# Kernel tuning notes

Measured on AMD Instinct MI355X. Metric: run time of the kernel, lower is better.

The kernel has to match this reference:

```python
import jax, jax.numpy as jnp
import numpy as np

N, F, H, C, E, G = 100000, 128, 64, 2, 1000000, 1000

def setup_inputs() -> dict:
    key = jax.random.key(0)
    ks = jax.random.split(key, 12)
    x = jax.random.normal(ks[0], (N, F), dtype=jnp.float32)
    edge_index = jax.random.randint(ks[1], (2, E), 0, N, dtype=jnp.int64)
    batch = jnp.sort(jax.random.randint(ks[2], (N,), 0, G, dtype=jnp.int64))
    def lin(k, fan_in, fan_out):
        s = 1.0 / np.sqrt(fan_in)
        kw, kb = jax.random.split(k)
        W = jax.random.uniform(kw, (fan_in, fan_out), jnp.float32, -s, s)
        b = jax.random.uniform(kb, (fan_out,), jnp.float32, -s, s)
        return W, b
    W1a, b1a = lin(ks[3], F, H)
    W1b, b1b = lin(ks[4], H, H)
    W2a, b2a = lin(ks[5], H, H)
    W2b, b2b = lin(ks[6], H, H)
    Wf, bf = lin(ks[7], H, C)
    return {"x": x, "edge_index": edge_index, "batch": batch,
            "W1a": W1a, "b1a": b1a, "W1b": W1b, "b1b": b1b,
            "W2a": W2a, "b2a": b2a, "W2b": W2b, "b2b": b2b,
            "Wf": Wf, "bf": bf}

def reference(x, edge_index, batch, W1a, b1a, W1b, b1b, W2a, b2a, W2b, b2b, Wf, bf):
    src, dst = edge_index[0], edge_index[1]
    n = x.shape[0]

    def gin_conv(h, Wa, ba, Wb, bb):
        # sum-aggregate source features onto destination nodes (eps = 0)
        agg = jax.ops.segment_sum(h[src], dst, num_segments=n)
        z = h + agg  # (1 + eps) * h + agg, eps=0
        return jax.nn.relu(z @ Wa + ba) @ Wb + bb

    h = jax.nn.relu(gin_conv(x, W1a, b1a, W1b, b1b))
    h = jax.nn.relu(gin_conv(h, W2a, b2a, W2b, b2b))

    # global mean pool per graph
    sums = jax.ops.segment_sum(h, batch, num_segments=G)
    counts = jax.ops.segment_sum(jnp.ones((n,), h.dtype), batch, num_segments=G)
    pooled = sums / jnp.clip(counts, 1.0)[:, None]
    return pooled @ Wf + bf
```

## Files before the change

### kernel.cpp

```cpp
#include <hip/hip_runtime.h>

#define HD 64
#define CAP 32


typedef _Float16 half8 __attribute__((ext_vector_type(8)));
typedef float f32x4 __attribute__((ext_vector_type(4)));

__device__ __forceinline__ unsigned short f2h(float f) {
    _Float16 h = (_Float16)f;
    unsigned short u;
    __builtin_memcpy(&u, &h, 2);
    return u;
}
__device__ __forceinline__ float h2f(unsigned short u) {
    _Float16 h;
    __builtin_memcpy(&h, &u, 2);
    return (float)h;
}

__device__ __forceinline__ int swz(int row, int bytecol) {
    return row * 128 + (bytecol ^ ((row & 7) << 4));
}
__device__ __forceinline__ int swz256(int row, int bytecol) {
    return row * 256 + (bytecol ^ ((row & 7) << 4));
}

__device__ __forceinline__ half8 bfrag(const float* __restrict__ W,
                                       int kc, int ntbase, int lane) {
    const int col = ntbase + (lane & 15);
    const float* wc = W + (size_t)(kc * 32 + ((lane >> 4) << 3)) * HD + col;
    half8 b;
#pragma unroll
    for (int j = 0; j < 8; ++j) b[j] = (_Float16)wc[j * HD];
    return b;
}

__global__ __launch_bounds__(128) void gemm128_mfma(const float* __restrict__ X,
                                                    const float* __restrict__ W,
                                                    unsigned short* __restrict__ Y, int n) {
    __shared__ __align__(16) unsigned short Xs[32 * 128];
    char* XsB = (char*)Xs;

    const int lane  = threadIdx.x & 63;
    const int wid   = threadIdx.x >> 6;
    const int row0  = blockIdx.x * 32;
    const int rbase = wid * 16;
    const int qo    = lane & 15;
    const int kg    = lane >> 4;

    const float4* Xg = (const float4*)X;
    for (int i = lane; i < 512; i += 64) {
        const int r   = i >> 5;
        const int c4  = i & 31;
        const int row = row0 + rbase + r;
        float4 v = make_float4(0.f, 0.f, 0.f, 0.f);
        if (row < n) v = Xg[(size_t)row * 32 + c4];
        ushort4 p;
        p.x = f2h(v.x); p.y = f2h(v.y); p.z = f2h(v.z); p.w = f2h(v.w);
        *(ushort4*)(XsB + swz256(rbase + r, c4 * 8)) = p;
    }

    const int arow = rbase + qo;
    half8 a[4];
#pragma unroll
    for (int kc = 0; kc < 4; ++kc)
        a[kc] = *(half8*)(XsB + swz256(arow, kc * 64 + kg * 16));

#pragma unroll
    for (int nt = 0; nt < 4; ++nt) {
        f32x4 c = (f32x4){0.f, 0.f, 0.f, 0.f};
#pragma unroll
        for (int kc = 0; kc < 4; ++kc)
            c = __builtin_amdgcn_mfma_f32_16x16x32_f16(a[kc], bfrag(W, kc, nt * 16, lane), c, 0, 0, 0);
#pragma unroll
        for (int j = 0; j < 4; ++j) {
            const int row = row0 + rbase + kg * 4 + j;
            if (row < n) Y[(size_t)row * HD + nt * 16 + qo] = f2h(c[j]);
        }
    }
}

__global__ __launch_bounds__(256) void fill_xcd(const int* __restrict__ src,
                                                const int* __restrict__ dst,
                                                int* __restrict__ fillpos,
                                                int* __restrict__ eidx,
                                                int E, int n) {
    const int xcd   = blockIdx.x & 7;
    const int chunk = blockIdx.x >> 3;
    const int nchk  = gridDim.x >> 3;
    const int cs    = (E + nchk - 1) / nchk;
    const int lo    = chunk * cs;
    const int hi    = min(lo + cs, E);
    const int nd8   = n >> 3;
    const int rlo   = xcd * nd8;
    const int rhi   = (xcd == 7) ? n : rlo + nd8;

    for (int t = lo + (int)threadIdx.x; t < hi; t += 256) {
        const int d = dst[t];
        if (d >= rlo && d < rhi) {
            const int p = atomicAdd(&fillpos[d], 1);
            if (p < CAP) eidx[(size_t)d * CAP + p] = src[t];
        }
    }
}

__device__ __forceinline__ void gather_pair(const unsigned short* __restrict__ Y,
                                            const int* __restrict__ deg,
                                            const int* __restrict__ eidx,
                                            int v0, int v1, int n, int lane,
                                            float4& A0, float4& A1) {
    const int sub = lane >> 4;
    const int qo  = lane & 15;
    const ushort4* Yq = (const ushort4*)Y;

    const int c0 = (v0 < n) ? min(deg[v0], CAP) : 0;
    const int c1 = (v1 < n) ? min(deg[v1], CAP) : 0;
    const int s0 = v0 * CAP;
    const int s1 = v1 * CAP;

    const int myu0 = (c0 > 0) ? eidx[s0 + min(lane, c0 - 1)] : 0;
    const int myu1 = (c1 > 0) ? eidx[s1 + min(lane, c1 - 1)] : 0;
    ushort4 self0 = make_ushort4(0, 0, 0, 0);
    ushort4 self1 = make_ushort4(0, 0, 0, 0);
    if (v0 < n && sub == 0) self0 = Yq[(size_t)v0 * 16 + qo];
    if (v1 < n && sub == 0) self1 = Yq[(size_t)v1 * 16 + qo];

    float4 a0 = make_float4(h2f(self0.x), h2f(self0.y), h2f(self0.z), h2f(self0.w));
    float4 a1 = make_float4(h2f(self1.x), h2f(self1.y), h2f(self1.z), h2f(self1.w));

    const int cmax = max(c0, c1);
#pragma unroll 1
    for (int i = 0; i < cmax; i += 16) {
        const int rem0 = c0 - i;
        const int rem1 = c1 - i;
        const int u00 = __shfl(myu0, i + 0  + sub);
        const int u01 = __shfl(myu0, i + 4  + sub);
        const int u02 = __shfl(myu0, i + 8  + sub);
        const int u03 = __shfl(myu0, i + 12 + sub);
        const int u10 = __shfl(myu1, i + 0  + sub);
        const int u11 = __shfl(myu1, i + 4  + sub);
        const int u12 = __shfl(myu1, i + 8  + sub);
        const int u13 = __shfl(myu1, i + 12 + sub);
        ushort4 f00 = make_ushort4(0,0,0,0), f01 = make_ushort4(0,0,0,0);
        ushort4 f02 = make_ushort4(0,0,0,0), f03 = make_ushort4(0,0,0,0);
        ushort4 f10 = make_ushort4(0,0,0,0), f11 = make_ushort4(0,0,0,0);
        ushort4 f12 = make_ushort4(0,0,0,0), f13 = make_ushort4(0,0,0,0);
        if (sub < rem0)      f00 = Yq[(size_t)u00 * 16 + qo];
        if (sub + 4 < rem0)  f01 = Yq[(size_t)u01 * 16 + qo];
        if (sub + 8 < rem0)  f02 = Yq[(size_t)u02 * 16 + qo];
        if (sub + 12 < rem0) f03 = Yq[(size_t)u03 * 16 + qo];
        if (sub < rem1)      f10 = Yq[(size_t)u10 * 16 + qo];
        if (sub + 4 < rem1)  f11 = Yq[(size_t)u11 * 16 + qo];
        if (sub + 8 < rem1)  f12 = Yq[(size_t)u12 * 16 + qo];
        if (sub + 12 < rem1) f13 = Yq[(size_t)u13 * 16 + qo];
        a0.x += (h2f(f00.x) + h2f(f01.x)) + (h2f(f02.x) + h2f(f03.x));
        a0.y += (h2f(f00.y) + h2f(f01.y)) + (h2f(f02.y) + h2f(f03.y));
        a0.z += (h2f(f00.z) + h2f(f01.z)) + (h2f(f02.z) + h2f(f03.z));
        a0.w += (h2f(f00.w) + h2f(f01.w)) + (h2f(f02.w) + h2f(f03.w));
        a1.x += (h2f(f10.x) + h2f(f11.x)) + (h2f(f12.x) + h2f(f13.x));
        a1.y += (h2f(f10.y) + h2f(f11.y)) + (h2f(f12.y) + h2f(f13.y));
        a1.z += (h2f(f10.z) + h2f(f11.z)) + (h2f(f12.z) + h2f(f13.z));
        a1.w += (h2f(f10.w) + h2f(f11.w)) + (h2f(f12.w) + h2f(f13.w));
    }

    a0.x += __shfl_xor(a0.x, 16); a0.y += __shfl_xor(a0.y, 16);
    a0.z += __shfl_xor(a0.z, 16); a0.w += __shfl_xor(a0.w, 16);
    a0.x += __shfl_xor(a0.x, 32); a0.y += __shfl_xor(a0.y, 32);
    a0.z += __shfl_xor(a0.z, 32); a0.w += __shfl_xor(a0.w, 32);
    a1.x += __shfl_xor(a1.x, 16); a1.y += __shfl_xor(a1.y, 16);
    a1.z += __shfl_xor(a1.z, 16); a1.w += __shfl_xor(a1.w, 16);
    a1.x += __shfl_xor(a1.x, 32); a1.y += __shfl_xor(a1.y, 32);
    a1.z += __shfl_xor(a1.z, 32); a1.w += __shfl_xor(a1.w, 32);
    A0 = a0;
    A1 = a1;
}

__global__ __launch_bounds__(128) void layer_mid(const unsigned short* __restrict__ Y,
                                                 const int* __restrict__ deg,
                                                 const int* __restrict__ eidx,
                                                 const float* __restrict__ bpre,
                                                 const float* __restrict__ Wb,
                                                 const float* __restrict__ bb,
                                                 const float* __restrict__ Wn,
                                                 unsigned short* __restrict__ Yout, int n) {
    __shared__ __align__(16) unsigned short Xs[32 * 64];
    char* XsB = (char*)Xs;

    const int lane  = threadIdx.x & 63;
    const int wid   = threadIdx.x >> 6;
    const int row0  = blockIdx.x * 32;
    const int rbase = wid * 16;
    const int qo    = lane & 15;
    const int kg    = lane >> 4;

    const float4 bp4 = ((const float4*)bpre)[qo];
#pragma unroll 1
    for (int rr = 0; rr < 16; rr += 2) {
        const int v0 = row0 + rbase + rr;
        float4 A0, A1;
        gather_pair(Y, deg, eidx, v0, v0 + 1, n, lane, A0, A1);
        if (lane < 16) {
            ushort4 p0, p1;
            p0.x = f2h(fmaxf(A0.x + bp4.x, 0.f));
            p0.y = f2h(fmaxf(A0.y + bp4.y, 0.f));
            p0.z = f2h(fmaxf(A0.z + bp4.z, 0.f));
            p0.w = f2h(fmaxf(A0.w + bp4.w, 0.f));
            p1.x = f2h(fmaxf(A1.x + bp4.x, 0.f));
            p1.y = f2h(fmaxf(A1.y + bp4.y, 0.f));
            p1.z = f2h(fmaxf(A1.z + bp4.z, 0.f));
            p1.w = f2h(fmaxf(A1.w + bp4.w, 0.f));
            *(ushort4*)(XsB + swz(rbase + rr, qo * 8)) = p0;
            *(ushort4*)(XsB + swz(rbase + rr + 1, qo * 8)) = p1;
        }
    }

    const int arow = rbase + qo;
    half8 a0 = *(half8*)(XsB + swz(arow, kg * 16));
    half8 a1 = *(half8*)(XsB + swz(arow, 64 + kg * 16));

    f32x4 acc[4];
#pragma unroll
    for (int nt = 0; nt < 4; ++nt) {
        acc[nt] = (f32x4){0.f, 0.f, 0.f, 0.f};
        acc[nt] = __builtin_amdgcn_mfma_f32_16x16x32_f16(a0, bfrag(Wb, 0, nt * 16, lane), acc[nt], 0, 0, 0);
        acc[nt] = __builtin_amdgcn_mfma_f32_16x16x32_f16(a1, bfrag(Wb, 1, nt * 16, lane), acc[nt], 0, 0, 0);
    }

#pragma unroll
    for (int nt = 0; nt < 4; ++nt) {
        const float bbv = bb[nt * 16 + qo];
#pragma unroll
        for (int j = 0; j < 4; ++j) {
            const float h = fmaxf(acc[nt][j] + bbv, 0.f);
            *(unsigned short*)(XsB + swz(rbase + kg * 4 + j, (nt * 16 + qo) * 2)) = f2h(h);
        }
    }

    a0 = *(half8*)(XsB + swz(arow, kg * 16));
    a1 = *(half8*)(XsB + swz(arow, 64 + kg * 16));

#pragma unroll
    for (int nt = 0; nt < 4; ++nt) {
        f32x4 c2 = (f32x4){0.f, 0.f, 0.f, 0.f};
        c2 = __builtin_amdgcn_mfma_f32_16x16x32_f16(a0, bfrag(Wn, 0, nt * 16, lane), c2, 0, 0, 0);
        c2 = __builtin_amdgcn_mfma_f32_16x16x32_f16(a1, bfrag(Wn, 1, nt * 16, lane), c2, 0, 0, 0);
#pragma unroll
        for (int j = 0; j < 4; ++j) {
            const int row = row0 + rbase + kg * 4 + j;
            if (row < n) Yout[(size_t)row * HD + nt * 16 + qo] = f2h(c2[j]);
        }
    }
}

__global__ __launch_bounds__(128) void layer_end(const unsigned short* __restrict__ Y,
                                                 const int* __restrict__ deg,
                                                 const int* __restrict__ eidx,
                                                 const float* __restrict__ bpre,
                                                 const float* __restrict__ Wb,
                                                 const float* __restrict__ bb,
                                                 const int* __restrict__ batch,
                                                 float* __restrict__ sums,
                                                 float* __restrict__ counts, int n) {
    __shared__ __align__(16) unsigned short Xs[32 * 64];
    char* XsB = (char*)Xs;

    const int lane  = threadIdx.x & 63;
    const int wid   = threadIdx.x >> 6;
    const int row0  = blockIdx.x * 32;
    const int rbase = wid * 16;
    const int qo    = lane & 15;
    const int kg    = lane >> 4;

    const float4 bp4 = ((const float4*)bpre)[qo];
#pragma unroll 1
    for (int rr = 0; rr < 16; rr += 2) {
        const int v0 = row0 + rbase + rr;
        float4 A0, A1;
        gather_pair(Y, deg, eidx, v0, v0 + 1, n, lane, A0, A1);
        if (lane < 16) {
            ushort4 p0, p1;
            p0.x = f2h(fmaxf(A0.x + bp4.x, 0.f));
            p0.y = f2h(fmaxf(A0.y + bp4.y, 0.f));
            p0.z = f2h(fmaxf(A0.z + bp4.z, 0.f));
            p0.w = f2h(fmaxf(A0.w + bp4.w, 0.f));
            p1.x = f2h(fmaxf(A1.x + bp4.x, 0.f));
            p1.y = f2h(fmaxf(A1.y + bp4.y, 0.f));
            p1.z = f2h(fmaxf(A1.z + bp4.z, 0.f));
            p1.w = f2h(fmaxf(A1.w + bp4.w, 0.f));
            *(ushort4*)(XsB + swz(rbase + rr, qo * 8)) = p0;
            *(ushort4*)(XsB + swz(rbase + rr + 1, qo * 8)) = p1;
        }
    }

    const int arow = rbase + qo;
    half8 a0 = *(half8*)(XsB + swz(arow, kg * 16));
    half8 a1 = *(half8*)(XsB + swz(arow, 64 + kg * 16));

#pragma unroll
    for (int nt = 0; nt < 4; ++nt) {
        f32x4 c = (f32x4){0.f, 0.f, 0.f, 0.f};
        c = __builtin_amdgcn_mfma_f32_16x16x32_f16(a0, bfrag(Wb, 0, nt * 16, lane), c, 0, 0, 0);
        c = __builtin_amdgcn_mfma_f32_16x16x32_f16(a1, bfrag(Wb, 1, nt * 16, lane), c, 0, 0, 0);
        const float bbv = bb[nt * 16 + qo];
#pragma unroll
        for (int j = 0; j < 4; ++j) {
            const float h = fmaxf(c[j] + bbv, 0.f);
            *(unsigned short*)(XsB + swz(rbase + kg * 4 + j, (nt * 16 + qo) * 2)) = f2h(h);
        }
    }

    const int vbase = row0 + rbase;
    int   curg = -1;
    float racc = 0.f;
    float rcnt = 0.f;
#pragma unroll 1
    for (int r = 0; r < 16; ++r) {
        const int v = vbase + r;
        int g = -1;
        if (v < n) g = batch[v];
        if (g != curg) {
            if (curg >= 0) {
                unsafeAtomicAdd(&sums[(size_t)curg * HD + lane], racc);
                if (lane == 0) unsafeAtomicAdd(&counts[curg], rcnt);
            }
            curg = g;
            racc = 0.f;
            rcnt = 0.f;
        }
        if (g >= 0) {
            racc += h2f(*(unsigned short*)(XsB + swz(rbase + r, lane * 2)));
            rcnt += 1.f;
        }
    }
    if (curg >= 0) {
        unsafeAtomicAdd(&sums[(size_t)curg * HD + lane], racc);
        if (lane == 0) unsafeAtomicAdd(&counts[curg], rcnt);
    }
}

__global__ __launch_bounds__(256) void final_linear(const float* __restrict__ sums,
                                                    const float* __restrict__ counts,
                                                    const float* __restrict__ Wf,
                                                    const float* __restrict__ bfv,
                                                    float* __restrict__ out, int G, int C) {
    const int t = blockIdx.x * 256 + threadIdx.x;
    if (t >= G * C) return;
    const int g = t / C;
    const int c = t - g * C;
    const float inv = 1.0f / fmaxf(counts[g], 1.0f);
    float acc = 0.f;
    for (int h = 0; h < HD; ++h) acc += sums[(size_t)g * HD + h] * Wf[h * C + c];
    out[t] = acc * inv + bfv[c];
}

extern "C" void kernel_launch(void* const* d_in, const int* in_sizes, int n_in,
                              void* d_out, int out_size, void* d_ws, size_t ws_size,
                              hipStream_t stream) {
    const float* x    = (const float*)d_in[0];
    const int*   ei   = (const int*)d_in[1];
    const int*   batc = (const int*)d_in[2];
    const float* W1a  = (const float*)d_in[3];
    const float* b1a  = (const float*)d_in[4];
    const float* W1b  = (const float*)d_in[5];
    const float* b1b  = (const float*)d_in[6];
    const float* W2a  = (const float*)d_in[7];
    const float* b2a  = (const float*)d_in[8];
    const float* W2b  = (const float*)d_in[9];
    const float* b2b  = (const float*)d_in[10];
    const float* Wf   = (const float*)d_in[11];
    const float* bfv  = (const float*)d_in[12];

    const int n = in_sizes[2];
    const int E = in_sizes[1] / 2;
    const int C = in_sizes[12];
    const int G = out_size / C;

    const int* src = ei;
    const int* dst = ei + E;

    unsigned short* yA = (unsigned short*)d_ws;
    unsigned short* yB = yA + (size_t)n * HD;
    float* sums    = (float*)(yB + (size_t)n * HD);
    float* counts  = sums + (size_t)G * HD;
    int*   fillpos = (int*)(counts + G);
    int*   eidx    = fillpos + n;

    const int layerGrid = (n + 31) / 32;
    const int NCHUNK    = 512;

    hipMemsetAsync(fillpos, 0, (size_t)n * sizeof(int), stream);
    fill_xcd<<<8 * NCHUNK, 256, 0, stream>>>(src, dst, fillpos, eidx, E, n);

    gemm128_mfma<<<layerGrid, 128, 0, stream>>>(x, W1a, yA, n);

    layer_mid<<<layerGrid, 128, 0, stream>>>(yA, fillpos, eidx,
                                             b1a, W1b, b1b, W2a, yB, n);

    hipMemsetAsync(sums, 0, (size_t)G * (HD + 1) * sizeof(float), stream);
    layer_end<<<layerGrid, 128, 0, stream>>>(yB, fillpos, eidx,
                                             b2a, W2b, b2b, batc, sums, counts, n);

    final_linear<<<(G * C + 255) / 256, 256, 0, stream>>>(sums, counts, Wf, bfv,
                                                          (float*)d_out, G, C);
}
```

Baseline: 158.8 us.

## Fuse edge fill, first GEMM and pool zeroing into one launch; gather four rows per wave

```diff
diff --git a/kernel.cpp b/kernel.cpp
--- a/kernel.cpp
+++ b/kernel.cpp
@@ -36,188 +36,191 @@
     return b;
 }
 
-__global__ __launch_bounds__(128) void gemm128_mfma(const float* __restrict__ X,
-                                                    const float* __restrict__ W,
-                                                    unsigned short* __restrict__ Y, int n) {
-    __shared__ __align__(16) unsigned short Xs[32 * 128];
+__global__ __launch_bounds__(256) void fused_pre(const int* __restrict__ src,
+                                                 const int* __restrict__ dst,
+                                                 int* __restrict__ fillpos,
+                                                 int* __restrict__ eidx, int E,
+                                                 const float* __restrict__ X,
+                                                 const float* __restrict__ W,
+                                                 unsigned short* __restrict__ Y, int n,
+                                                 float* __restrict__ zbuf, int ZN,
+                                                 int FB, int GB, int ZB) {
+    __shared__ __align__(16) unsigned short Xs[64 * 128];
     char* XsB = (char*)Xs;
 
-    const int lane  = threadIdx.x & 63;
-    const int wid   = threadIdx.x >> 6;
-    const int row0  = blockIdx.x * 32;
-    const int rbase = wid * 16;
-    const int qo    = lane & 15;
-    const int kg    = lane >> 4;
-
-    const float4* Xg = (const float4*)X;
-    for (int i = lane; i < 512; i += 64) {
-        const int r   = i >> 5;
-        const int c4  = i & 31;
-        const int row = row0 + rbase + r;
-        float4 v = make_float4(0.f, 0.f, 0.f, 0.f);
-        if (row < n) v = Xg[(size_t)row * 32 + c4];
-        ushort4 p;
-        p.x = f2h(v.x); p.y = f2h(v.y); p.z = f2h(v.z); p.w = f2h(v.w);
-        *(ushort4*)(XsB + swz256(rbase + r, c4 * 8)) = p;
-    }
-
-    const int arow = rbase + qo;
-    half8 a[4];
-#pragma unroll
-    for (int kc = 0; kc < 4; ++kc)
-        a[kc] = *(half8*)(XsB + swz256(arow, kc * 64 + kg * 16));
-
-#pragma unroll
-    for (int nt = 0; nt < 4; ++nt) {
-        f32x4 c = (f32x4){0.f, 0.f, 0.f, 0.f};
+    const int bid = blockIdx.x;
+    const int tid = threadIdx.x;
+
+    if (bid < FB) {
+        const int xcd   = bid & 7;
+        const int chunk = bid >> 3;
+        const int nchk  = FB >> 3;
+        const int cs    = (E + nchk - 1) / nchk;
+        const int lo    = chunk * cs;
+        const int hi    = min(lo + cs, E);
+        const int nd8   = n >> 3;
+        const int rlo   = xcd * nd8;
+        const int rhi   = (xcd == 7) ? n : rlo + nd8;
+
+        for (int t = lo + tid; t < hi; t += 256) {
+            const int d = dst[t];
+            if (d >= rlo && d < rhi) {
+                const int p = atomicAdd(&fillpos[d], 1);
+                if (p < CAP) eidx[(size_t)d * CAP + p] = src[t];
+            }
+        }
+        return;
+    }
+
+    if (bid < FB + GB) {
+        const int lane  = tid & 63;
+        const int wid   = tid >> 6;
+        const int row0  = (bid - FB) * 64;
+        const int rbase = wid * 16;
+        const int qo    = lane & 15;
+        const int kg    = lane >> 4;
+
+        const float4* Xg = (const float4*)X;
+        for (int i = lane; i < 512; i += 64) {
+            const int r   = i >> 5;
+            const int c4  = i & 31;
+            const int row = row0 + rbase + r;
+            float4 v = make_float4(0.f, 0.f, 0.f, 0.f);
+            if (row < n) v = Xg[(size_t)row * 32 + c4];
+            ushort4 p;
+            p.x = f2h(v.x); p.y = f2h(v.y); p.z = f2h(v.z); p.w = f2h(v.w);
+            *(ushort4*)(XsB + swz256(rbase + r, c4 * 8)) = p;
+        }
+
+        const int arow = rbase + qo;
+        half8 a[4];
 #pragma unroll
         for (int kc = 0; kc < 4; ++kc)
-            c = __builtin_amdgcn_mfma_f32_16x16x32_f16(a[kc], bfrag(W, kc, nt * 16, lane), c, 0, 0, 0);
-#pragma unroll
-        for (int j = 0; j < 4; ++j) {
-            const int row = row0 + rbase + kg * 4 + j;
-            if (row < n) Y[(size_t)row * HD + nt * 16 + qo] = f2h(c[j]);
-        }
-    }
-}
-
-__global__ __launch_bounds__(256) void fill_xcd(const int* __restrict__ src,
-                                                const int* __restrict__ dst,
-                                                int* __restrict__ fillpos,
-                                                int* __restrict__ eidx,
-                                                int E, int n) {
-    const int xcd   = blockIdx.x & 7;
-    const int chunk = blockIdx.x >> 3;
-    const int nchk  = gridDim.x >> 3;
-    const int cs    = (E + nchk - 1) / nchk;
-    const int lo    = chunk * cs;
-    const int hi    = min(lo + cs, E);
-    const int nd8   = n >> 3;
-    const int rlo   = xcd * nd8;
-    const int rhi   = (xcd == 7) ? n : rlo + nd8;
-
-    for (int t = lo + (int)threadIdx.x; t < hi; t += 256) {
-        const int d = dst[t];
-        if (d >= rlo && d < rhi) {
-            const int p = atomicAdd(&fillpos[d], 1);
-            if (p < CAP) eidx[(size_t)d * CAP + p] = src[t];
-        }
-    }
-}
-
-__device__ __forceinline__ void gather_pair(const unsigned short* __restrict__ Y,
-                                            const int* __restrict__ deg,
-                                            const int* __restrict__ eidx,
-                                            int v0, int v1, int n, int lane,
-                                            float4& A0, float4& A1) {
+            a[kc] = *(half8*)(XsB + swz256(arow, kc * 64 + kg * 16));
+
+#pragma unroll
+        for (int nt = 0; nt < 4; ++nt) {
+            f32x4 c = (f32x4){0.f, 0.f, 0.f, 0.f};
+#pragma unroll
+            for (int kc = 0; kc < 4; ++kc)
+                c = __builtin_amdgcn_mfma_f32_16x16x32_f16(a[kc], bfrag(W, kc, nt * 16, lane), c, 0, 0, 0);
+#pragma unroll
+            for (int j = 0; j < 4; ++j) {
+                const int row = row0 + rbase + kg * 4 + j;
+                if (row < n) Y[(size_t)row * HD + nt * 16 + qo] = f2h(c[j]);
+            }
+        }
+        return;
+    }
+
+    {
+        const int zb   = bid - FB - GB;
+        const int strd = ZB * 256;
+        for (int i = zb * 256 + tid; i < ZN; i += strd) zbuf[i] = 0.f;
+    }
+}
+
+__device__ __forceinline__ void gather_quad4(const unsigned short* __restrict__ Y,
+                                             const int* __restrict__ deg,
+                                             const int* __restrict__ eidx,
+                                             int v0, int n, int lane,
+                                             float4 A[4]) {
     const int sub = lane >> 4;
     const int qo  = lane & 15;
     const ushort4* Yq = (const ushort4*)Y;
 
-    const int c0 = (v0 < n) ? min(deg[v0], CAP) : 0;
-    const int c1 = (v1 < n) ? min(deg[v1], CAP) : 0;
-    const int s0 = v0 * CAP;
-    const int s1 = v1 * CAP;
-
-    const int myu0 = (c0 > 0) ? eidx[s0 + min(lane, c0 - 1)] : 0;
-    const int myu1 = (c1 > 0) ? eidx[s1 + min(lane, c1 - 1)] : 0;
-    ushort4 self0 = make_ushort4(0, 0, 0, 0);
-    ushort4 self1 = make_ushort4(0, 0, 0, 0);
-    if (v0 < n && sub == 0) self0 = Yq[(size_t)v0 * 16 + qo];
-    if (v1 < n && sub == 0) self1 = Yq[(size_t)v1 * 16 + qo];
-
-    float4 a0 = make_float4(h2f(self0.x), h2f(self0.y), h2f(self0.z), h2f(self0.w));
-    float4 a1 = make_float4(h2f(self1.x), h2f(self1.y), h2f(self1.z), h2f(self1.w));
-
-    const int cmax = max(c0, c1);
+    int c[4], myu[4];
+#pragma unroll
+    for (int r = 0; r < 4; ++r)
+        c[r] = (v0 + r < n) ? min(deg[v0 + r], CAP) : 0;
+#pragma unroll
+    for (int r = 0; r < 4; ++r)
+        myu[r] = (c[r] > 0) ? eidx[(v0 + r) * CAP + min(lane, c[r] - 1)] : 0;
+
+    ushort4 self[4];
+#pragma unroll
+    for (int r = 0; r < 4; ++r) {
+        self[r] = make_ushort4(0, 0, 0, 0);
+        if (v0 + r < n && sub == 0) self[r] = Yq[(size_t)(v0 + r) * 16 + qo];
+    }
+#pragma unroll
+    for (int r = 0; r < 4; ++r)
+        A[r] = make_float4(h2f(self[r].x), h2f(self[r].y), h2f(self[r].z), h2f(self[r].w));
+
+    const int cmax = max(max(c[0], c[1]), max(c[2], c[3]));
 #pragma unroll 1
     for (int i = 0; i < cmax; i += 16) {
-        const int rem0 = c0 - i;
-        const int rem1 = c1 - i;
-        const int u00 = __shfl(myu0, i + 0  + sub);
-        const int u01 = __shfl(myu0, i + 4  + sub);
-        const int u02 = __shfl(myu0, i + 8  + sub);
-        const int u03 = __shfl(myu0, i + 12 + sub);
-        const int u10 = __shfl(myu1, i + 0  + sub);
-        const int u11 = __shfl(myu1, i + 4  + sub);
-        const int u12 = __shfl(myu1, i + 8  + sub);
-        const int u13 = __shfl(myu1, i + 12 + sub);
-        ushort4 f00 = make_ushort4(0,0,0,0), f01 = make_ushort4(0,0,0,0);
-        ushort4 f02 = make_ushort4(0,0,0,0), f03 = make_ushort4(0,0,0,0);
-        ushort4 f10 = make_ushort4(0,0,0,0), f11 = make_ushort4(0,0,0,0);
-        ushort4 f12 = make_ushort4(0,0,0,0), f13 = make_ushort4(0,0,0,0);
-        if (sub < rem0)      f00 = Yq[(size_t)u00 * 16 + qo];
-        if (sub + 4 < rem0)  f01 = Yq[(size_t)u01 * 16 + qo];
-        if (sub + 8 < rem0)  f02 = Yq[(size_t)u02 * 16 + qo];
-        if (sub + 12 < rem0) f03 = Yq[(size_t)u03 * 16 + qo];
-        if (sub < rem1)      f10 = Yq[(size_t)u10 * 16 + qo];
-        if (sub + 4 < rem1)  f11 = Yq[(size_t)u11 * 16 + qo];
-        if (sub + 8 < rem1)  f12 = Yq[(size_t)u12 * 16 + qo];
-        if (sub + 12 < rem1) f13 = Yq[(size_t)u13 * 16 + qo];
-        a0.x += (h2f(f00.x) + h2f(f01.x)) + (h2f(f02.x) + h2f(f03.x));
-        a0.y += (h2f(f00.y) + h2f(f01.y)) + (h2f(f02.y) + h2f(f03.y));
-        a0.z += (h2f(f00.z) + h2f(f01.z)) + (h2f(f02.z) + h2f(f03.z));
-        a0.w += (h2f(f00.w) + h2f(f01.w)) + (h2f(f02.w) + h2f(f03.w));
-        a1.x += (h2f(f10.x) + h2f(f11.x)) + (h2f(f12.x) + h2f(f13.x));
-        a1.y += (h2f(f10.y) + h2f(f11.y)) + (h2f(f12.y) + h2f(f13.y));
-        a1.z += (h2f(f10.z) + h2f(f11.z)) + (h2f(f12.z) + h2f(f13.z));
-        a1.w += (h2f(f10.w) + h2f(f11.w)) + (h2f(f12.w) + h2f(f13.w));
-    }
-
-    a0.x += __shfl_xor(a0.x, 16); a0.y += __shfl_xor(a0.y, 16);
-    a0.z += __shfl_xor(a0.z, 16); a0.w += __shfl_xor(a0.w, 16);
-    a0.x += __shfl_xor(a0.x, 32); a0.y += __shfl_xor(a0.y, 32);
-    a0.z += __shfl_xor(a0.z, 32); a0.w += __shfl_xor(a0.w, 32);
-    a1.x += __shfl_xor(a1.x, 16); a1.y += __shfl_xor(a1.y, 16);
-    a1.z += __shfl_xor(a1.z, 16); a1.w += __shfl_xor(a1.w, 16);
-    a1.x += __shfl_xor(a1.x, 32); a1.y += __shfl_xor(a1.y, 32);
-    a1.z += __shfl_xor(a1.z, 32); a1.w += __shfl_xor(a1.w, 32);
-    A0 = a0;
-    A1 = a1;
-}
-
-__global__ __launch_bounds__(128) void layer_mid(const unsigned short* __restrict__ Y,
-                                                 const int* __restrict__ deg,
-                                                 const int* __restrict__ eidx,
-                                                 const float* __restrict__ bpre,
-                                                 const float* __restrict__ Wb,
-                                                 const float* __restrict__ bb,
-                                                 const float* __restrict__ Wn,
-                                                 unsigned short* __restrict__ Yout, int n) {
-    __shared__ __align__(16) unsigned short Xs[32 * 64];
+        ushort4 f[4][4];
+        int u[4][4];
+#pragma unroll
+        for (int r = 0; r < 4; ++r) {
+#pragma unroll
+            for (int j = 0; j < 4; ++j) {
+                u[r][j] = __shfl(myu[r], i + j * 4 + sub);
+                f[r][j] = make_ushort4(0, 0, 0, 0);
+            }
+        }
+#pragma unroll
+        for (int r = 0; r < 4; ++r) {
+            const int rem = c[r] - i;
+#pragma unroll
+            for (int j = 0; j < 4; ++j)
+                if (sub + j * 4 < rem) f[r][j] = Yq[(size_t)u[r][j] * 16 + qo];
+        }
+#pragma unroll
+        for (int r = 0; r < 4; ++r) {
+            A[r].x += (h2f(f[r][0].x) + h2f(f[r][1].x)) + (h2f(f[r][2].x) + h2f(f[r][3].x));
+            A[r].y += (h2f(f[r][0].y) + h2f(f[r][1].y)) + (h2f(f[r][2].y) + h2f(f[r][3].y));
+            A[r].z += (h2f(f[r][0].z) + h2f(f[r][1].z)) + (h2f(f[r][2].z) + h2f(f[r][3].z));
+            A[r].w += (h2f(f[r][0].w) + h2f(f[r][1].w)) + (h2f(f[r][2].w) + h2f(f[r][3].w));
+        }
+    }
+
+#pragma unroll
+    for (int r = 0; r < 4; ++r) {
+        A[r].x += __shfl_xor(A[r].x, 16); A[r].y += __shfl_xor(A[r].y, 16);
+        A[r].z += __shfl_xor(A[r].z, 16); A[r].w += __shfl_xor(A[r].w, 16);
+        A[r].x += __shfl_xor(A[r].x, 32); A[r].y += __shfl_xor(A[r].y, 32);
+        A[r].z += __shfl_xor(A[r].z, 32); A[r].w += __shfl_xor(A[r].w, 32);
+    }
+}
+
+__global__ __launch_bounds__(64) void layer_mid(const unsigned short* __restrict__ Y,
+                                                const int* __restrict__ deg,
+                                                const int* __restrict__ eidx,
+                                                const float* __restrict__ bpre,
+                                                const float* __restrict__ Wb,
+                                                const float* __restrict__ bb,
+                                                const float* __restrict__ Wn,
+                                                unsigned short* __restrict__ Yout, int n) {
+    __shared__ __align__(16) unsigned short Xs[16 * 64];
     char* XsB = (char*)Xs;
 
-    const int lane  = threadIdx.x & 63;
-    const int wid   = threadIdx.x >> 6;
-    const int row0  = blockIdx.x * 32;
-    const int rbase = wid * 16;
-    const int qo    = lane & 15;
-    const int kg    = lane >> 4;
+    const int lane = threadIdx.x;
+    const int row0 = blockIdx.x * 16;
+    const int qo   = lane & 15;
+    const int kg   = lane >> 4;
 
     const float4 bp4 = ((const float4*)bpre)[qo];
 #pragma unroll 1
-    for (int rr = 0; rr < 16; rr += 2) {
-        const int v0 = row0 + rbase + rr;
-        float4 A0, A1;
-        gather_pair(Y, deg, eidx, v0, v0 + 1, n, lane, A0, A1);
+    for (int rr = 0; rr < 16; rr += 4) {
+        float4 A[4];
+        gather_quad4(Y, deg, eidx, row0 + rr, n, lane, A);
         if (lane < 16) {
-            ushort4 p0, p1;
-            p0.x = f2h(fmaxf(A0.x + bp4.x, 0.f));
-            p0.y = f2h(fmaxf(A0.y + bp4.y, 0.f));
-            p0.z = f2h(fmaxf(A0.z + bp4.z, 0.f));
-            p0.w = f2h(fmaxf(A0.w + bp4.w, 0.f));
-            p1.x = f2h(fmaxf(A1.x + bp4.x, 0.f));
-            p1.y = f2h(fmaxf(A1.y + bp4.y, 0.f));
-            p1.z = f2h(fmaxf(A1.z + bp4.z, 0.f));
-            p1.w = f2h(fmaxf(A1.w + bp4.w, 0.f));
-            *(ushort4*)(XsB + swz(rbase + rr, qo * 8)) = p0;
-            *(ushort4*)(XsB + swz(rbase + rr + 1, qo * 8)) = p1;
-        }
-    }
-
-    const int arow = rbase + qo;
-    half8 a0 = *(half8*)(XsB + swz(arow, kg * 16));
-    half8 a1 = *(half8*)(XsB + swz(arow, 64 + kg * 16));
+#pragma unroll
+            for (int r = 0; r < 4; ++r) {
+                ushort4 p;
+                p.x = f2h(fmaxf(A[r].x + bp4.x, 0.f));
+                p.y = f2h(fmaxf(A[r].y + bp4.y, 0.f));
+                p.z = f2h(fmaxf(A[r].z + bp4.z, 0.f));
+                p.w = f2h(fmaxf(A[r].w + bp4.w, 0.f));
+                *(ushort4*)(XsB + swz(rr + r, qo * 8)) = p;
+            }
+        }
+    }
+
+    half8 a0 = *(half8*)(XsB + swz(qo, kg * 16));
+    half8 a1 = *(half8*)(XsB + swz(qo, 64 + kg * 16));
 
     f32x4 acc[4];
 #pragma unroll
@@ -233,12 +236,12 @@
 #pragma unroll
         for (int j = 0; j < 4; ++j) {
             const float h = fmaxf(acc[nt][j] + bbv, 0.f);
-            *(unsigned short*)(XsB + swz(rbase + kg * 4 + j, (nt * 16 + qo) * 2)) = f2h(h);
-        }
-    }
-
-    a0 = *(half8*)(XsB + swz(arow, kg * 16));
-    a1 = *(half8*)(XsB + swz(arow, 64 + kg * 16));
+            *(unsigned short*)(XsB + swz(kg * 4 + j, (nt * 16 + qo) * 2)) = f2h(h);
+        }
+    }
+
+    a0 = *(half8*)(XsB + swz(qo, kg * 16));
+    a1 = *(half8*)(XsB + swz(qo, 64 + kg * 16));
 
 #pragma unroll
     for (int nt = 0; nt < 4; ++nt) {
@@ -247,55 +250,49 @@
         c2 = __builtin_amdgcn_mfma_f32_16x16x32_f16(a1, bfrag(Wn, 1, nt * 16, lane), c2, 0, 0, 0);
 #pragma unroll
         for (int j = 0; j < 4; ++j) {
-            const int row = row0 + rbase + kg * 4 + j;
+            const int row = row0 + kg * 4 + j;
             if (row < n) Yout[(size_t)row * HD + nt * 16 + qo] = f2h(c2[j]);
         }
     }
 }
 
-__global__ __launch_bounds__(128) void layer_end(const unsigned short* __restrict__ Y,
-                                                 const int* __restrict__ deg,
-                                                 const int* __restrict__ eidx,
-                                                 const float* __restrict__ bpre,
-                                                 const float* __restrict__ Wb,
-                                                 const float* __restrict__ bb,
-                                                 const int* __restrict__ batch,
-                                                 float* __restrict__ sums,
-                                                 float* __restrict__ counts, int n) {
-    __shared__ __align__(16) unsigned short Xs[32 * 64];
+__global__ __launch_bounds__(64) void layer_end(const unsigned short* __restrict__ Y,
+                                                const int* __restrict__ deg,
+                                                const int* __restrict__ eidx,
+                                                const float* __restrict__ bpre,
+                                                const float* __restrict__ Wb,
+                                                const float* __restrict__ bb,
+                                                const int* __restrict__ batch,
+                                                float* __restrict__ sums,
+                                                float* __restrict__ counts, int n) {
+    __shared__ __align__(16) unsigned short Xs[16 * 64];
     char* XsB = (char*)Xs;
 
-    const int lane  = threadIdx.x & 63;
-    const int wid   = threadIdx.x >> 6;
-    const int row0  = blockIdx.x * 32;
-    const int rbase = wid * 16;
-    const int qo    = lane & 15;
-    const int kg    = lane >> 4;
+    const int lane = threadIdx.x;
+    const int row0 = blockIdx.x * 16;
+    const int qo   = lane & 15;
+    const int kg   = lane >> 4;
 
     const float4 bp4 = ((const float4*)bpre)[qo];
 #pragma unroll 1
-    for (int rr = 0; rr < 16; rr += 2) {
-        const int v0 = row0 + rbase + rr;
-        float4 A0, A1;
-        gather_pair(Y, deg, eidx, v0, v0 + 1, n, lane, A0, A1);
+    for (int rr = 0; rr < 16; rr += 4) {
+        float4 A[4];
+        gather_quad4(Y, deg, eidx, row0 + rr, n, lane, A);
         if (lane < 16) {
-            ushort4 p0, p1;
-            p0.x = f2h(fmaxf(A0.x + bp4.x, 0.f));
-            p0.y = f2h(fmaxf(A0.y + bp4.y, 0.f));
-            p0.z = f2h(fmaxf(A0.z + bp4.z, 0.f));
-            p0.w = f2h(fmaxf(A0.w + bp4.w, 0.f));
-            p1.x = f2h(fmaxf(A1.x + bp4.x, 0.f));
-            p1.y = f2h(fmaxf(A1.y + bp4.y, 0.f));
-            p1.z = f2h(fmaxf(A1.z + bp4.z, 0.f));
-            p1.w = f2h(fmaxf(A1.w + bp4.w, 0.f));
-            *(ushort4*)(XsB + swz(rbase + rr, qo * 8)) = p0;
-            *(ushort4*)(XsB + swz(rbase + rr + 1, qo * 8)) = p1;
-        }
-    }
-
-    const int arow = rbase + qo;
-    half8 a0 = *(half8*)(XsB + swz(arow, kg * 16));
-    half8 a1 = *(half8*)(XsB + swz(arow, 64 + kg * 16));
+#pragma unroll
+            for (int r = 0; r < 4; ++r) {
+                ushort4 p;
+                p.x = f2h(fmaxf(A[r].x + bp4.x, 0.f));
+                p.y = f2h(fmaxf(A[r].y + bp4.y, 0.f));
+                p.z = f2h(fmaxf(A[r].z + bp4.z, 0.f));
+                p.w = f2h(fmaxf(A[r].w + bp4.w, 0.f));
+                *(ushort4*)(XsB + swz(rr + r, qo * 8)) = p;
+            }
+        }
+    }
+
+    half8 a0 = *(half8*)(XsB + swz(qo, kg * 16));
+    half8 a1 = *(half8*)(XsB + swz(qo, 64 + kg * 16));
 
 #pragma unroll
     for (int nt = 0; nt < 4; ++nt) {
@@ -306,17 +303,16 @@
 #pragma unroll
         for (int j = 0; j < 4; ++j) {
             const float h = fmaxf(c[j] + bbv, 0.f);
-            *(unsigned short*)(XsB + swz(rbase + kg * 4 + j, (nt * 16 + qo) * 2)) = f2h(h);
-        }
-    }
-
-    const int vbase = row0 + rbase;
+            *(unsigned short*)(XsB + swz(kg * 4 + j, (nt * 16 + qo) * 2)) = f2h(h);
+        }
+    }
+
     int   curg = -1;
     float racc = 0.f;
     float rcnt = 0.f;
 #pragma unroll 1
     for (int r = 0; r < 16; ++r) {
-        const int v = vbase + r;
+        const int v = row0 + r;
         int g = -1;
         if (v < n) g = batch[v];
         if (g != curg) {
@@ -329,7 +325,7 @@
             rcnt = 0.f;
         }
         if (g >= 0) {
-            racc += h2f(*(unsigned short*)(XsB + swz(rbase + r, lane * 2)));
+            racc += h2f(*(unsigned short*)(XsB + swz(r, lane * 2)));
             rcnt += 1.f;
         }
     }
@@ -386,20 +382,23 @@
     int*   fillpos = (int*)(counts + G);
     int*   eidx    = fillpos + n;
 
-    const int layerGrid = (n + 31) / 32;
-    const int NCHUNK    = 512;
+    const int layerGrid = (n + 15) / 16;
+    const int FB = 8 * 512;
+    const int GB = (n + 63) / 64;
+    const int ZB = 32;
+    const int ZN = G * (HD + 1);
 
     hipMemsetAsync(fillpos, 0, (size_t)n * sizeof(int), stream);
-    fill_xcd<<<8 * NCHUNK, 256, 0, stream>>>(src, dst, fillpos, eidx, E, n);
-
-    gemm128_mfma<<<layerGrid, 128, 0, stream>>>(x, W1a, yA, n);
-
-    layer_mid<<<layerGrid, 128, 0, stream>>>(yA, fillpos, eidx,
-                                             b1a, W1b, b1b, W2a, yB, n);
-
-    hipMemsetAsync(sums, 0, (size_t)G * (HD + 1) * sizeof(float), stream);
-    layer_end<<<layerGrid, 128, 0, stream>>>(yB, fillpos, eidx,
-                                             b2a, W2b, b2b, batc, sums, counts, n);
+
+    fused_pre<<<FB + GB + ZB, 256, 0, stream>>>(src, dst, fillpos, eidx, E,
+                                                x, W1a, yA, n,
+                                                sums, ZN, FB, GB, ZB);
+
+    layer_mid<<<layerGrid, 64, 0, stream>>>(yA, fillpos, eidx,
+                                            b1a, W1b, b1b, W2a, yB, n);
+
+    layer_end<<<layerGrid, 64, 0, stream>>>(yB, fillpos, eidx,
+                                            b2a, W2b, b2b, batc, sums, counts, n);
 
     final_linear<<<(G * C + 255) / 256, 256, 0, stream>>>(sums, counts, Wf, bfv,
                                                           (float*)d_out, G, C);
```

Result: slower. 198.1 us (+24.7%).
